# Kernel optimization log

Measured on AMD Instinct MI355X. Metric: run time of the kernel, lower is better.

## Reference

```python
import jax, jax.numpy as jnp
import numpy as np

EMB = 2048
H = 16        # num query heads
G = 4         # num kv groups (kv heads)
GS = H // G   # group size = 4
HD = EMB // H # head dim = 128
B, T = 2, 2048


def setup_inputs() -> dict:
    key = jax.random.key(0)
    ks = jax.random.split(key, 6)
    s = 1.0 / np.sqrt(EMB)
    return {
        "x": jax.random.normal(ks[0], (B, T, EMB), dtype=jnp.float32),
        "Wq": jax.random.normal(ks[1], (EMB, EMB), dtype=jnp.float32) * s,
        "Wk": jax.random.normal(ks[2], (EMB, EMB), dtype=jnp.float32) * s,
        "Wv": jax.random.normal(ks[3], (EMB, EMB), dtype=jnp.float32) * s,
        "Wp": jax.random.normal(ks[4], (EMB, EMB), dtype=jnp.float32) * s,
        "bp": jnp.zeros((EMB,), dtype=jnp.float32),
    }


def reference(x, Wq, Wk, Wv, Wp, bp):
    # Dropout layers (p=0.5) treated as identity (eval mode) for a deterministic baseline.
    b, t, c = x.shape
    # torch nn.Linear: y = x @ W.T
    q = (x @ Wq.T).reshape(b, t, G, GS, HD)          # head h = g*GS + s
    q = q.transpose(0, 2, 3, 1, 4)                   # (B, G, GS, T, HD)
    # GQA: keys/values use only the first head of each group, then broadcast
    # over the GS query heads of that group (equivalent to repeat_interleave).
    k = (x @ Wk.T).reshape(b, t, G, GS, HD)[:, :, :, 0, :].transpose(0, 2, 1, 3)  # (B, G, T, HD)
    v = (x @ Wv.T).reshape(b, t, G, GS, HD)[:, :, :, 0, :].transpose(0, 2, 1, 3)  # (B, G, T, HD)

    scale = HD ** (-0.5)
    scores = jnp.einsum('bgsqd,bgkd->bgsqk', q, k) * scale  # (B,G,GS,T,T)
    causal = jnp.tril(jnp.ones((t, t), dtype=bool))
    scores = jnp.where(causal, scores, -jnp.inf)
    attn = jax.nn.softmax(scores, axis=-1)
    out = jnp.einsum('bgsqk,bgkd->bgsqd', attn, v)           # (B,G,GS,T,HD)
    out = out.transpose(0, 3, 1, 2, 4).reshape(b, t, c)       # heads back in h=g*GS+s order
    return out @ Wp.T + bp
```

## Files before the change

### kernel.cpp

```cpp
#include <hip/hip_runtime.h>
#include <hip/hip_bf16.h>


typedef unsigned short ushort_t;
typedef __bf16 bf16x8 __attribute__((ext_vector_type(8)));
typedef float f32x4 __attribute__((ext_vector_type(4)));

__device__ __forceinline__ ushort_t f2bf(float f) {
  union { float f; unsigned u; } x; x.f = f;
  unsigned r = x.u + 0x7fffu + ((x.u >> 16) & 1u);
  return (ushort_t)(r >> 16);
}

__global__ __launch_bounds__(256) void cast4(const float* __restrict__ in,
                                             ushort_t* __restrict__ out) {
  int i = blockIdx.x * 256 + threadIdx.x;
  float4 v = reinterpret_cast<const float4*>(in)[i];
  ushort4 o;
  o.x = f2bf(v.x); o.y = f2bf(v.y); o.z = f2bf(v.z); o.w = f2bf(v.w);
  reinterpret_cast<ushort4*>(out)[i] = o;
}

__global__ __launch_bounds__(256) void cast_compact(const float* __restrict__ in,
                                                    ushort_t* __restrict__ out) {
  int i = blockIdx.x * 256 + threadIdx.x;
  int row = i >> 9, c = i & 511;
  int srow = ((row >> 7) << 9) | (row & 127);
  float4 v = reinterpret_cast<const float4*>(in + (size_t)srow * 2048)[c];
  ushort4 o;
  o.x = f2bf(v.x); o.y = f2bf(v.y); o.z = f2bf(v.z); o.w = f2bf(v.w);
  reinterpret_cast<ushort4*>(out + (size_t)row * 2048)[c] = o;
}

template<bool FINAL>
__global__ __launch_bounds__(256) void gemm_bt(const ushort_t* __restrict__ A,
                                               const ushort_t* __restrict__ B,
                                               ushort_t* __restrict__ Cb,
                                               float* __restrict__ Cf,
                                               const float* __restrict__ bias,
                                               int M, int N, int K) {
  __shared__ ushort_t lA[128 * 32];
  __shared__ ushort_t lB[128 * 32];
  const int lane = threadIdx.x & 63;
  const int w = threadIdx.x >> 6;
  const int m0 = blockIdx.y * 128;
  const int n0 = blockIdx.x * 128;
  const int wm = (w >> 1) * 64, wn = (w & 1) * 64;
  const int l4 = lane >> 4, l15 = lane & 15;

  const f32x4 zero = {0.f, 0.f, 0.f, 0.f};
  f32x4 acc[4][4];
#pragma unroll
  for (int i = 0; i < 4; ++i)
#pragma unroll
    for (int j = 0; j < 4; ++j) acc[i][j] = zero;

  const int srow = w * 16 + (lane >> 2);
  const int scol = (lane & 3) * 8;
  const ushort_t* ga = A + (size_t)(m0 + srow) * K + scol;
  const ushort_t* gb = B + (size_t)(n0 + srow) * K + scol;

  for (int kt = 0; kt < K; kt += 32) {
#pragma unroll
    for (int i = 0; i < 2; ++i) {
      __builtin_amdgcn_global_load_lds(
          (const __attribute__((address_space(1))) void*)(ga + (size_t)i * 64 * K + kt),
          (__attribute__((address_space(3))) void*)(&lA[w * 512 + i * 2048]), 16, 0, 0);
      __builtin_amdgcn_global_load_lds(
          (const __attribute__((address_space(1))) void*)(gb + (size_t)i * 64 * K + kt),
          (__attribute__((address_space(3))) void*)(&lB[w * 512 + i * 2048]), 16, 0, 0);
    }
    __syncthreads();
    bf16x8 af[4], bfr[4];
#pragma unroll
    for (int t = 0; t < 4; ++t) {
      af[t]  = *reinterpret_cast<const bf16x8*>(&lA[(wm + t * 16 + l15) * 32 + l4 * 8]);
      bfr[t] = *reinterpret_cast<const bf16x8*>(&lB[(wn + t * 16 + l15) * 32 + l4 * 8]);
    }
#pragma unroll
    for (int mi = 0; mi < 4; ++mi)
#pragma unroll
      for (int ni = 0; ni < 4; ++ni)
        acc[mi][ni] = __builtin_amdgcn_mfma_f32_16x16x32_bf16(af[mi], bfr[ni],
                                                              acc[mi][ni], 0, 0, 0);
    __syncthreads();
  }

#pragma unroll
  for (int mi = 0; mi < 4; ++mi)
#pragma unroll
    for (int ni = 0; ni < 4; ++ni) {
      int row = m0 + wm + mi * 16 + l4 * 4;
      int col = n0 + wn + ni * 16 + l15;
#pragma unroll
      for (int r = 0; r < 4; ++r) {
        float v = acc[mi][ni][r];
        if (FINAL) Cf[(size_t)(row + r) * N + col] = v + bias[col];
        else       Cb[(size_t)(row + r) * N + col] = f2bf(v);
      }
    }
}

__global__ __launch_bounds__(256, 2) void attn_kernel(const ushort_t* __restrict__ Qb, int ldQ,
                                                      const ushort_t* __restrict__ Kb, int ldK,
                                                      const ushort_t* __restrict__ Vt,
                                                      ushort_t* __restrict__ Ob) {
  __shared__ ushort_t ldsK[2][64 * 128];
  __shared__ ushort_t ldsV[2][128 * 64];
  __shared__ ushort_t pbuf[4][16 * 72];

  const int lane = threadIdx.x & 63;
  const int w = threadIdx.x >> 6;
  const int swz = ((blockIdx.x & 7) << 6) | (blockIdx.x >> 3);
  const int b = swz >> 8, hq = (swz >> 4) & 15, pair = swz & 15;
  const int g = hq >> 2;
  const int l4 = lane >> 4, l15 = lane & 15;
  const int tau_hi = 31 - pair, tau_lo = pair;
  const int hi_iters = tau_hi + 1;
  const int total_iters = hi_iters + tau_lo + 1;
  const float C = 0.12751744f;

  const int krow = w * 4 + (lane >> 4);
  const ushort_t* kBase = Kb + (size_t)(b * 2048 + krow) * ldK + g * 128 + ((lane & 15) ^ (krow & 7)) * 8;
  const int vrow = w * 8 + (lane >> 3);
  const ushort_t* vBase = Vt + (size_t)(g * 128 + vrow) * 4096 + b * 2048 + ((lane & 7) ^ (vrow & 7)) * 8;

  const f32x4 zero = {0.f, 0.f, 0.f, 0.f};
  f32x4 o[8];
  float mr[4], lr[4];
  bf16x8 qf[4];

  auto LOADQ = [&](int tau) {
    const ushort_t* qp = Qb + (size_t)(b * 2048 + tau * 64 + w * 16 + l15) * ldQ + hq * 128 + l4 * 8;
#pragma unroll
    for (int kk = 0; kk < 4; ++kk) {
      bf16x8 q = *reinterpret_cast<const bf16x8*>(qp + kk * 32);
#pragma unroll
      for (int j = 0; j < 8; ++j) q[j] = (__bf16)((float)q[j] * C);
      qf[kk] = q;
    }
  };
  auto RESET = [&]() {
#pragma unroll
    for (int i = 0; i < 8; ++i) o[i] = zero;
#pragma unroll
    for (int r = 0; r < 4; ++r) { mr[r] = -3.0e38f; lr[r] = 0.f; }
  };
  auto STAGE = [&](int tt, int bc) {
    const int js = (tt < hi_iters) ? tt * 64 : (tt - hi_iters) * 64;
    const ushort_t* ks = kBase + (size_t)js * ldK;
    const ushort_t* vs = vBase + js;
#pragma unroll
    for (int i = 0; i < 4; ++i) {
      __builtin_amdgcn_global_load_lds(
          (const __attribute__((address_space(1))) void*)(ks + (size_t)i * 16 * ldK),
          (__attribute__((address_space(3))) void*)(&ldsK[bc][i * 2048 + w * 512]), 16, 0, 0);
      __builtin_amdgcn_global_load_lds(
          (const __attribute__((address_space(1))) void*)(vs + (size_t)i * 32 * 4096),
          (__attribute__((address_space(3))) void*)(&ldsV[bc][i * 2048 + w * 512]), 16, 0, 0);
    }
  };
  auto FINALIZE = [&](int tau) {
#pragma unroll
    for (int r = 0; r < 4; ++r) {
#pragma unroll
      for (int d = 1; d < 16; d <<= 1) lr[r] += __shfl_xor(lr[r], d, 16);
      lr[r] = 1.0f / lr[r];
    }
    ushort_t* op = Ob + (size_t)(b * 2048 + tau * 64 + w * 16) * 2048 + hq * 128;
#pragma unroll
    for (int ni = 0; ni < 8; ++ni)
#pragma unroll
      for (int r = 0; r < 4; ++r)
        op[(size_t)(l4 * 4 + r) * 2048 + ni * 16 + l15] = f2bf(o[ni][r] * lr[r]);
  };

  RESET();
  LOADQ(tau_hi);
  STAGE(0, 0);

  for (int t = 0; t < total_iters; ++t) {
    if (t == hi_iters) {
      FINALIZE(tau_hi);
      RESET();
      LOADQ(tau_lo);
    }
    __syncthreads();
    if (t + 1 < total_iters) STAGE(t + 1, (t + 1) & 1);
    const int bc = t & 1;

    const int tau = (t < hi_iters) ? tau_hi : tau_lo;
    const int tloc = (t < hi_iters) ? t : (t - hi_iters);
    const int j0 = tloc * 64;
    const int q0 = tau * 64 + w * 16;
    const bool diag = (tloc == tau);

    f32x4 s[4];
#pragma unroll
    for (int i = 0; i < 4; ++i) s[i] = zero;
#pragma unroll
    for (int ni = 0; ni < 4; ++ni) {
      const int R = ni * 16 + l15;
#pragma unroll
      for (int kk = 0; kk < 4; ++kk) {
        bf16x8 kf = *reinterpret_cast<const bf16x8*>(
            &ldsK[bc][R * 128 + ((kk * 4 + l4) ^ (R & 7)) * 8]);
        s[ni] = __builtin_amdgcn_mfma_f32_16x16x32_bf16(qf[kk], kf, s[ni], 0, 0, 0);
      }
    }
    float pmax[4] = {-3.0e38f, -3.0e38f, -3.0e38f, -3.0e38f};
    if (diag) {
#pragma unroll
      for (int ni = 0; ni < 4; ++ni) {
        int col = j0 + ni * 16 + l15;
#pragma unroll
        for (int r = 0; r < 4; ++r) {
          int qq = q0 + l4 * 4 + r;
          float v = (col <= qq) ? s[ni][r] : -3.0e38f;
          s[ni][r] = v;
          pmax[r] = fmaxf(pmax[r], v);
        }
      }
    } else {
#pragma unroll
      for (int ni = 0; ni < 4; ++ni)
#pragma unroll
        for (int r = 0; r < 4; ++r) pmax[r] = fmaxf(pmax[r], s[ni][r]);
    }
    bool small = (pmax[0] <= mr[0] + 8.f) & (pmax[1] <= mr[1] + 8.f) &
                 (pmax[2] <= mr[2] + 8.f) & (pmax[3] <= mr[3] + 8.f);
    if (!__all(small)) {
#pragma unroll
      for (int r = 0; r < 4; ++r) {
#pragma unroll
        for (int d = 1; d < 16; d <<= 1) pmax[r] = fmaxf(pmax[r], __shfl_xor(pmax[r], d, 16));
        float mn = fmaxf(mr[r], pmax[r]);
        float corr = exp2f(mr[r] - mn);
        mr[r] = mn;
        lr[r] *= corr;
#pragma unroll
        for (int i = 0; i < 8; ++i) o[i][r] *= corr;
      }
    }
#pragma unroll
    for (int ni = 0; ni < 4; ++ni)
#pragma unroll
      for (int r = 0; r < 4; ++r) {
        float p = exp2f(s[ni][r] - mr[r]);
        lr[r] += p;
        pbuf[w][(l4 * 4 + r) * 72 + ni * 16 + l15] = f2bf(p);
      }
    bf16x8 pa[2];
#pragma unroll
    for (int kk2 = 0; kk2 < 2; ++kk2)
      pa[kk2] = *reinterpret_cast<const bf16x8*>(&pbuf[w][l15 * 72 + kk2 * 32 + l4 * 8]);
#pragma unroll
    for (int ni = 0; ni < 8; ++ni) {
      const int R = ni * 16 + l15;
#pragma unroll
      for (int kk2 = 0; kk2 < 2; ++kk2) {
        bf16x8 vf = *reinterpret_cast<const bf16x8*>(
            &ldsV[bc][R * 64 + ((kk2 * 4 + l4) ^ (R & 7)) * 8]);
        o[ni] = __builtin_amdgcn_mfma_f32_16x16x32_bf16(pa[kk2], vf, o[ni], 0, 0, 0);
      }
    }
  }
  FINALIZE(tau_lo);
}

extern "C" void kernel_launch(void* const* d_in, const int* in_sizes, int n_in,
                              void* d_out, int out_size, void* d_ws, size_t ws_size,
                              hipStream_t stream) {
  const float* x  = (const float*)d_in[0];
  const float* Wq = (const float*)d_in[1];
  const float* Wk = (const float*)d_in[2];
  const float* Wv = (const float*)d_in[3];
  const float* Wp = (const float*)d_in[4];
  const float* bp = (const float*)d_in[5];
  float* out = (float*)d_out;

  char* ws = (char*)d_ws;
  size_t off = 0;
  ushort_t* xb    = (ushort_t*)(ws + off); off += (size_t)4096 * 2048 * 2;
  ushort_t* wqkb  = (ushort_t*)(ws + off); off += (size_t)2560 * 2048 * 2;
  ushort_t* wvb   = (ushort_t*)(ws + off); off += (size_t)512 * 2048 * 2;
  ushort_t* wpb   = (ushort_t*)(ws + off); off += (size_t)2048 * 2048 * 2;
  ushort_t* qkbuf = (ushort_t*)(ws + off); off += (size_t)4096 * 2560 * 2;
  ushort_t* vtb   = (ushort_t*)(ws + off); off += (size_t)512 * 4096 * 2;
  ushort_t* obuf  = (ushort_t*)(ws + off); off += (size_t)4096 * 2048 * 2;

  cast4<<<8192, 256, 0, stream>>>(x, xb);
  cast4<<<4096, 256, 0, stream>>>(Wq, wqkb);
  cast_compact<<<1024, 256, 0, stream>>>(Wk, wqkb + (size_t)2048 * 2048);
  cast_compact<<<1024, 256, 0, stream>>>(Wv, wvb);
  cast4<<<4096, 256, 0, stream>>>(Wp, wpb);

  gemm_bt<false><<<dim3(20, 32), 256, 0, stream>>>(xb, wqkb, qkbuf, nullptr, nullptr,
                                                   4096, 2560, 2048);
  gemm_bt<false><<<dim3(32, 4), 256, 0, stream>>>(wvb, xb, vtb, nullptr, nullptr,
                                                  512, 4096, 2048);

  attn_kernel<<<512, 256, 0, stream>>>(qkbuf, 2560, qkbuf + 2048, 2560, vtb, obuf);

  gemm_bt<true><<<dim3(16, 32), 256, 0, stream>>>(obuf, wpb, nullptr, out, bp,
                                                  4096, 2048, 2048);
}
```

Measured before the change: 376.1 us.

## Merge cast launches, fuse QK/V projections, deepen GEMM K-tile with swizzled LDS

The five fp32-to-bf16 cast launches become one kernel, and the two projection GEMMs (QK and transposed V) become one launch of 768 blocks. The shared GEMM tile now loads a 64-wide K slab per iteration instead of 32, which halves the barrier count, and it XOR-swizzles LDS columns to avoid bank conflicts on fragment reads. In exchange LDS per block doubles, which may lower occupancy, and the larger slab is still single-buffered.

```diff
diff --git a/kernel.cpp b/kernel.cpp
--- a/kernel.cpp
+++ b/kernel.cpp
@@ -12,18 +12,15 @@
   return (ushort_t)(r >> 16);
 }
 
-__global__ __launch_bounds__(256) void cast4(const float* __restrict__ in,
-                                             ushort_t* __restrict__ out) {
-  int i = blockIdx.x * 256 + threadIdx.x;
+__device__ __forceinline__ void cast_plain(const float* __restrict__ in,
+                                           ushort_t* __restrict__ out, int i) {
   float4 v = reinterpret_cast<const float4*>(in)[i];
   ushort4 o;
   o.x = f2bf(v.x); o.y = f2bf(v.y); o.z = f2bf(v.z); o.w = f2bf(v.w);
   reinterpret_cast<ushort4*>(out)[i] = o;
 }
-
-__global__ __launch_bounds__(256) void cast_compact(const float* __restrict__ in,
-                                                    ushort_t* __restrict__ out) {
-  int i = blockIdx.x * 256 + threadIdx.x;
+__device__ __forceinline__ void cast_cmp(const float* __restrict__ in,
+                                         ushort_t* __restrict__ out, int i) {
   int row = i >> 9, c = i & 511;
   int srow = ((row >> 7) << 9) | (row & 127);
   float4 v = reinterpret_cast<const float4*>(in + (size_t)srow * 2048)[c];
@@ -31,20 +28,34 @@
   o.x = f2bf(v.x); o.y = f2bf(v.y); o.z = f2bf(v.z); o.w = f2bf(v.w);
   reinterpret_cast<ushort4*>(out + (size_t)row * 2048)[c] = o;
 }
+__global__ __launch_bounds__(256) void cast_all(const float* __restrict__ x,
+                                                const float* __restrict__ Wq,
+                                                const float* __restrict__ Wk,
+                                                const float* __restrict__ Wv,
+                                                const float* __restrict__ Wp,
+                                                ushort_t* __restrict__ xb,
+                                                ushort_t* __restrict__ wqkb,
+                                                ushort_t* __restrict__ wvb,
+                                                ushort_t* __restrict__ wpb) {
+  int bid = blockIdx.x, tid = threadIdx.x;
+  if (bid < 8192)       cast_plain(x,  xb,  bid * 256 + tid);
+  else if (bid < 12288) cast_plain(Wq, wqkb, (bid - 8192) * 256 + tid);
+  else if (bid < 16384) cast_plain(Wp, wpb, (bid - 12288) * 256 + tid);
+  else if (bid < 17408) cast_cmp(Wk, wqkb + (size_t)2048 * 2048, (bid - 16384) * 256 + tid);
+  else                  cast_cmp(Wv, wvb, (bid - 17408) * 256 + tid);
+}
 
 template<bool FINAL>
-__global__ __launch_bounds__(256) void gemm_bt(const ushort_t* __restrict__ A,
-                                               const ushort_t* __restrict__ B,
-                                               ushort_t* __restrict__ Cb,
-                                               float* __restrict__ Cf,
-                                               const float* __restrict__ bias,
-                                               int M, int N, int K) {
-  __shared__ ushort_t lA[128 * 32];
-  __shared__ ushort_t lB[128 * 32];
+__device__ __forceinline__ void gemm_tile(ushort_t* __restrict__ lA,
+                                          ushort_t* __restrict__ lB,
+                                          const ushort_t* __restrict__ A,
+                                          const ushort_t* __restrict__ B,
+                                          ushort_t* __restrict__ Cb,
+                                          float* __restrict__ Cf,
+                                          const float* __restrict__ bias,
+                                          int m0, int n0, int N, int K) {
   const int lane = threadIdx.x & 63;
   const int w = threadIdx.x >> 6;
-  const int m0 = blockIdx.y * 128;
-  const int n0 = blockIdx.x * 128;
   const int wm = (w >> 1) * 64, wn = (w & 1) * 64;
   const int l4 = lane >> 4, l15 = lane & 15;
 
@@ -55,34 +66,39 @@
 #pragma unroll
     for (int j = 0; j < 4; ++j) acc[i][j] = zero;
 
-  const int srow = w * 16 + (lane >> 2);
-  const int scol = (lane & 3) * 8;
+  const int srow = w * 8 + (lane >> 3);
+  const int scol = ((lane & 7) ^ (lane >> 3)) * 8;
   const ushort_t* ga = A + (size_t)(m0 + srow) * K + scol;
   const ushort_t* gb = B + (size_t)(n0 + srow) * K + scol;
 
-  for (int kt = 0; kt < K; kt += 32) {
-#pragma unroll
-    for (int i = 0; i < 2; ++i) {
+  for (int kt = 0; kt < K; kt += 64) {
+#pragma unroll
+    for (int i = 0; i < 4; ++i) {
       __builtin_amdgcn_global_load_lds(
-          (const __attribute__((address_space(1))) void*)(ga + (size_t)i * 64 * K + kt),
-          (__attribute__((address_space(3))) void*)(&lA[w * 512 + i * 2048]), 16, 0, 0);
+          (const __attribute__((address_space(1))) void*)(ga + (size_t)i * 32 * K + kt),
+          (__attribute__((address_space(3))) void*)(&lA[i * 2048 + w * 512]), 16, 0, 0);
       __builtin_amdgcn_global_load_lds(
-          (const __attribute__((address_space(1))) void*)(gb + (size_t)i * 64 * K + kt),
-          (__attribute__((address_space(3))) void*)(&lB[w * 512 + i * 2048]), 16, 0, 0);
+          (const __attribute__((address_space(1))) void*)(gb + (size_t)i * 32 * K + kt),
+          (__attribute__((address_space(3))) void*)(&lB[i * 2048 + w * 512]), 16, 0, 0);
     }
     __syncthreads();
-    bf16x8 af[4], bfr[4];
-#pragma unroll
-    for (int t = 0; t < 4; ++t) {
-      af[t]  = *reinterpret_cast<const bf16x8*>(&lA[(wm + t * 16 + l15) * 32 + l4 * 8]);
-      bfr[t] = *reinterpret_cast<const bf16x8*>(&lB[(wn + t * 16 + l15) * 32 + l4 * 8]);
-    }
-#pragma unroll
-    for (int mi = 0; mi < 4; ++mi)
-#pragma unroll
-      for (int ni = 0; ni < 4; ++ni)
-        acc[mi][ni] = __builtin_amdgcn_mfma_f32_16x16x32_bf16(af[mi], bfr[ni],
-                                                              acc[mi][ni], 0, 0, 0);
+#pragma unroll
+    for (int kk = 0; kk < 2; ++kk) {
+      bf16x8 af[4], bfr[4];
+#pragma unroll
+      for (int t = 0; t < 4; ++t) {
+        const int Ra = wm + t * 16 + l15;
+        const int Rb = wn + t * 16 + l15;
+        af[t]  = *reinterpret_cast<const bf16x8*>(&lA[Ra * 64 + ((kk * 4 + l4) ^ (Ra & 7)) * 8]);
+        bfr[t] = *reinterpret_cast<const bf16x8*>(&lB[Rb * 64 + ((kk * 4 + l4) ^ (Rb & 7)) * 8]);
+      }
+#pragma unroll
+      for (int mi = 0; mi < 4; ++mi)
+#pragma unroll
+        for (int ni = 0; ni < 4; ++ni)
+          acc[mi][ni] = __builtin_amdgcn_mfma_f32_16x16x32_bf16(af[mi], bfr[ni],
+                                                                acc[mi][ni], 0, 0, 0);
+    }
     __syncthreads();
   }
 
@@ -99,6 +115,34 @@
         else       Cb[(size_t)(row + r) * N + col] = f2bf(v);
       }
     }
+}
+
+__global__ __launch_bounds__(256) void proj_fused(const ushort_t* __restrict__ xb,
+                                                  const ushort_t* __restrict__ wqkb,
+                                                  const ushort_t* __restrict__ wvb,
+                                                  ushort_t* __restrict__ qkbuf,
+                                                  ushort_t* __restrict__ vtb) {
+  __shared__ ushort_t lA[128 * 64];
+  __shared__ ushort_t lB[128 * 64];
+  int bid = blockIdx.x;
+  if (bid < 640) {
+    gemm_tile<false>(lA, lB, xb, wqkb, qkbuf, nullptr, nullptr,
+                     (bid / 20) * 128, (bid % 20) * 128, 2560, 2048);
+  } else {
+    int t = bid - 640;
+    gemm_tile<false>(lA, lB, wvb, xb, vtb, nullptr, nullptr,
+                     (t / 32) * 128, (t % 32) * 128, 4096, 2048);
+  }
+}
+
+__global__ __launch_bounds__(256) void gemm_final(const ushort_t* __restrict__ A,
+                                                  const ushort_t* __restrict__ B,
+                                                  float* __restrict__ Cf,
+                                                  const float* __restrict__ bias) {
+  __shared__ ushort_t lA[128 * 64];
+  __shared__ ushort_t lB[128 * 64];
+  gemm_tile<true>(lA, lB, A, B, nullptr, Cf, bias,
+                  (int)blockIdx.y * 128, (int)blockIdx.x * 128, 2048, 2048);
 }
 
 __global__ __launch_bounds__(256, 2) void attn_kernel(const ushort_t* __restrict__ Qb, int ldQ,
@@ -289,19 +333,11 @@
   ushort_t* vtb   = (ushort_t*)(ws + off); off += (size_t)512 * 4096 * 2;
   ushort_t* obuf  = (ushort_t*)(ws + off); off += (size_t)4096 * 2048 * 2;
 
-  cast4<<<8192, 256, 0, stream>>>(x, xb);
-  cast4<<<4096, 256, 0, stream>>>(Wq, wqkb);
-  cast_compact<<<1024, 256, 0, stream>>>(Wk, wqkb + (size_t)2048 * 2048);
-  cast_compact<<<1024, 256, 0, stream>>>(Wv, wvb);
-  cast4<<<4096, 256, 0, stream>>>(Wp, wpb);
-
-  gemm_bt<false><<<dim3(20, 32), 256, 0, stream>>>(xb, wqkb, qkbuf, nullptr, nullptr,
-                                                   4096, 2560, 2048);
-  gemm_bt<false><<<dim3(32, 4), 256, 0, stream>>>(wvb, xb, vtb, nullptr, nullptr,
-                                                  512, 4096, 2048);
+  cast_all<<<18432, 256, 0, stream>>>(x, Wq, Wk, Wv, Wp, xb, wqkb, wvb, wpb);
+
+  proj_fused<<<768, 256, 0, stream>>>(xb, wqkb, wvb, qkbuf, vtb);
 
   attn_kernel<<<512, 256, 0, stream>>>(qkbuf, 2560, qkbuf + 2048, 2560, vtb, obuf);
 
-  gemm_bt<true><<<dim3(16, 32), 256, 0, stream>>>(obuf, wpb, nullptr, out, bp,
-                                                  4096, 2048, 2048);
-}
+  gemm_final<<<dim3(16, 32), 256, 0, stream>>>(obuf, wpb, out, bp);
+}
```

Result: faster. 307.3 us (-18.3%).
